# Kernel tuning notes

Measured on AMD Instinct MI355X. Metric: run time of the kernel, lower is better.

The kernel has to match this reference:

```python
import jax, jax.numpy as jnp
import numpy as np

NUM_HEADS = 12


def setup_inputs() -> dict:
    key = jax.random.key(0)
    k1, k2, k3, k4, k5 = jax.random.split(key, 5)
    B, N, C = 64, 197, 768
    P = 10  # prefix length
    H, D = NUM_HEADS, C // NUM_HEADS
    return {
        "x": jax.random.normal(k1, (B, N, C), dtype=jnp.float32),
        "prompt": jax.random.normal(k2, (B, 2, P, H, D), dtype=jnp.float32),
        "qkv_w": jax.random.normal(k3, (3 * C, C), dtype=jnp.float32) * 0.02,
        "proj_w": jax.random.normal(k4, (C, C), dtype=jnp.float32) * 0.02,
        "proj_b": jax.random.normal(k5, (C,), dtype=jnp.float32) * 0.02,
    }


def reference(x, prompt, qkv_w, proj_w, proj_b):
    B, N, C = x.shape
    H = NUM_HEADS
    D = C // H
    scale = D ** -0.5

    # qkv projection (no bias), split into per-head q, k, v: [B, H, N, D]
    qkv = jnp.einsum("bnc,fc->bnf", x, qkv_w)              # [B, N, 3C]
    qkv = qkv.reshape(B, N, 3, H, D).transpose(2, 0, 3, 1, 4)
    q, k, v = qkv[0], qkv[1], qkv[2]

    # prompt: [B, 2, P, H, D] -> [2, B, H, P, D]; concat prefix onto k, v
    p = prompt.transpose(1, 0, 3, 2, 4)
    k = jnp.concatenate([p[0], k], axis=2)                  # [B, H, P+N, D]
    v = jnp.concatenate([p[1], v], axis=2)

    attn = jnp.einsum("bhnd,bhmd->bhnm", q, k) * scale      # [B, H, N, P+N]
    attn = jax.nn.softmax(attn, axis=-1)                    # attn_drop p=0 -> identity

    out = jnp.einsum("bhnm,bhmd->bhnd", attn, v)            # [B, H, N, D]
    out = out.transpose(0, 2, 1, 3).reshape(B, N, C)
    out = jnp.einsum("bnc,oc->bno", out, proj_w) + proj_b   # proj_drop p=0 -> identity
    return out
```

## Files before the change

### kernel.cpp

```cpp
#include <hip/hip_runtime.h>
#include <hip/hip_bf16.h>
#include <stdint.h>

#define NH 12
#define DH 64
#define CC 768
#define NTOK 197
#define PFX 10
#define MKV 207
#define BB 64
#define MROWS (BB * NTOK)
#define MPAD (99 * 128)
#define NT_QKV 9
#define MT_QKV 50
#define MPAD2 (MT_QKV * 256)
#define KV_PAD 208
#define KV_PAD2 224
#define VSTRIDE 232

typedef __attribute__((__ext_vector_type__(8))) short bf16x8;
typedef __attribute__((__ext_vector_type__(4))) float f32x4;

__device__ __forceinline__ ushort f2bf(float f) {
    union { float f; uint32_t u; } x; x.f = f;
    uint32_t u = x.u;
    return (ushort)((u + 0x7fffu + ((u >> 16) & 1u)) >> 16);
}

__device__ __forceinline__ void gload_lds16(const void* g, void* l) {
    __builtin_amdgcn_global_load_lds(
        (const __attribute__((address_space(1))) void*)g,
        (__attribute__((address_space(3))) void*)l, 16, 0, 0);
}

__device__ __forceinline__ int xcd_chunked(int orig, int nwg) {
    int q = nwg >> 3, r = nwg & 7;
    int xcd = orig & 7, rem = orig >> 3;
    return (xcd < r ? xcd * (q + 1) : r * (q + 1) + (xcd - r) * q) + rem;
}

__global__ void cvt_bf16(const float* __restrict__ src, ushort* __restrict__ dst, int n4) {
    int i = blockIdx.x * 256 + threadIdx.x;
    if (i >= n4) return;
    float4 v = reinterpret_cast<const float4*>(src)[i];
    ushort4 o = make_ushort4(f2bf(v.x), f2bf(v.y), f2bf(v.z), f2bf(v.w));
    reinterpret_cast<ushort4*>(dst)[i] = o;
}

__global__ void prompt_scatter(const float* __restrict__ prompt,
                               ushort* __restrict__ kbuf, ushort* __restrict__ vt) {
    int i = blockIdx.x * 256 + threadIdx.x;
    if (i >= BB * 2 * PFX * NH * DH) return;
    int d = i & 63;
    int h = (i >> 6) % NH;
    int p = (i / (64 * NH)) % PFX;
    int s = (i / (64 * NH * PFX)) & 1;
    int b = i / (64 * NH * PFX * 2);
    ushort val = f2bf(prompt[i]);
    int bh = b * NH + h;
    if (s == 0) kbuf[(bh * KV_PAD + p) * DH + d] = val;
    else        vt[(bh * DH + d) * KV_PAD2 + p] = val;
}

#define STAGE6(kt) {                                                              \
    const int bsel = (kt) & 1; const int koff = (kt) * 64;                        \
    gload_lds16(pA[0] + koff, &lds[bsel][0][0 * 4096 + w * 512]);                 \
    gload_lds16(pA[2] + koff, &lds[bsel][0][2 * 4096 + w * 512]);                 \
    gload_lds16(pB[0] + koff, &lds[bsel][1][0 * 4096 + w * 512]);                 \
    gload_lds16(pB[1] + koff, &lds[bsel][1][1 * 4096 + w * 512]);                 \
    gload_lds16(pB[2] + koff, &lds[bsel][1][2 * 4096 + w * 512]);                 \
    gload_lds16(pB[3] + koff, &lds[bsel][1][3 * 4096 + w * 512]); }

#define STAGE2(kt) {                                                              \
    const int bsel = (kt) & 1; const int koff = (kt) * 64;                        \
    gload_lds16(pA[1] + koff, &lds[bsel][0][1 * 4096 + w * 512]);                 \
    gload_lds16(pA[3] + koff, &lds[bsel][0][3 * 4096 + w * 512]); }

#define PHASE(t, p, VMSTR, DOSTAGE) {                                             \
    if (DOSTAGE) { if ((p) == 0) STAGE6((t) + 1) else STAGE2((t) + 1) }           \
    asm volatile("s_waitcnt vmcnt(" VMSTR ")" ::: "memory");                      \
    __builtin_amdgcn_s_barrier();                                                 \
    __builtin_amdgcn_sched_barrier(0);                                            \
    const ushort* Ab = &lds[(t) & 1][0][0];                                       \
    const ushort* Bb = &lds[(t) & 1][1][0];                                       \
    bf16x8 af[4][2], bf[4][2];                                                    \
    _Pragma("unroll") for (int i = 0; i < 4; ++i)                                 \
      _Pragma("unroll") for (int ks = 0; ks < 2; ++ks)                            \
        af[i][ks] = *reinterpret_cast<const bf16x8*>(                             \
            &Ab[(wm * 128 + ((p) * 4 + i) * 16 + lr) * 64 + coff[ks]]);           \
    _Pragma("unroll") for (int n = 0; n < 4; ++n)                                 \
      _Pragma("unroll") for (int ks = 0; ks < 2; ++ks)                            \
        bf[n][ks] = *reinterpret_cast<const bf16x8*>(                             \
            &Bb[(wn * 64 + n * 16 + lr) * 64 + coff[ks]]);                        \
    __builtin_amdgcn_s_setprio(1);                                                \
    _Pragma("unroll") for (int ks = 0; ks < 2; ++ks)                              \
      _Pragma("unroll") for (int i = 0; i < 4; ++i)                               \
        _Pragma("unroll") for (int n = 0; n < 4; ++n)                             \
          acc[(p) * 4 + i][n] = __builtin_amdgcn_mfma_f32_16x16x32_bf16(          \
              af[i][ks], bf[n][ks], acc[(p) * 4 + i][n], 0, 0, 0);                \
    __builtin_amdgcn_s_setprio(0);                                                \
    __builtin_amdgcn_s_barrier();                                                 \
    __builtin_amdgcn_sched_barrier(0);                                            \
}

__global__ __launch_bounds__(512, 2) void gemm_qkv8(const ushort* __restrict__ A,
                                                    const ushort* __restrict__ Bw,
                                                    ushort* __restrict__ qbuf,
                                                    ushort* __restrict__ kbuf,
                                                    ushort* __restrict__ vt) {
    __shared__ __align__(16) ushort lds[2][2][256 * 64];
    const int tid  = threadIdx.x;
    const int lane = tid & 63;
    const int w    = tid >> 6;
    const int wm = w >> 2, wn = w & 3;
    const int g = lane >> 4, lr = lane & 15;
    const int wgid = xcd_chunked(blockIdx.x, gridDim.x);
    const int row0 = (wgid / NT_QKV) * 256;
    const int col0 = (wgid % NT_QKV) * 256;

    const int sr  = tid >> 3;
    const int scb = (((tid & 7) ^ ((tid >> 3) & 7)) << 3);
    const int lr7 = lr & 7;
    int coff[2];
    coff[0] = ((0 * 4 + g) ^ lr7) << 3;
    coff[1] = ((1 * 4 + g) ^ lr7) << 3;

    const ushort* pA[4];
    #pragma unroll
    for (int q = 0; q < 4; ++q)
        pA[q] = A + (size_t)(row0 + q * 64 + sr) * CC + scb;
    const ushort* pB[4];
    #pragma unroll
    for (int j = 0; j < 4; ++j)
        pB[j] = Bw + (size_t)(col0 + j * 64 + sr) * CC + scb;

    f32x4 acc[8][4] = {};

    STAGE6(0)
    STAGE2(0)

    for (int t = 0; t < 11; ++t) {
        PHASE(t, 0, "8", true)
        PHASE(t, 1, "8", true)
    }
    PHASE(11, 0, "2", false)
    PHASE(11, 1, "0", false)

    #pragma unroll
    for (int ni = 0; ni < 4; ++ni) {
        int f = col0 + wn * 64 + ni * 16 + lr;
        int s   = f / CC;
        int rem = f - s * CC;
        int h = rem >> 6, d = rem & 63;
        #pragma unroll
        for (int mi = 0; mi < 8; ++mi) {
            #pragma unroll
            for (int rr = 0; rr < 4; ++rr) {
                int r = row0 + wm * 128 + mi * 16 + g * 4 + rr;
                if (r >= MROWS) continue;
                int b = r / NTOK;
                int n = r - b * NTOK;
                ushort val = f2bf(acc[mi][ni][rr]);
                int bh = b * NH + h;
                if (s == 0)      qbuf[(bh * KV_PAD + n) * DH + d] = val;
                else if (s == 1) kbuf[(bh * KV_PAD + n + PFX) * DH + d] = val;
                else             vt[(bh * DH + d) * KV_PAD2 + n + PFX] = val;
            }
        }
    }
}

#define GEMM_PRE(A_, B_, KDIM, NTILES)                                               \
    __shared__ __align__(16) ushort Alds0[128 * 32];                                 \
    __shared__ __align__(16) ushort Blds0[128 * 32];                                 \
    __shared__ __align__(16) ushort Alds1[128 * 32];                                 \
    __shared__ __align__(16) ushort Blds1[128 * 32];                                 \
    const int tid  = threadIdx.x;                                                    \
    const int lane = tid & 63;                                                       \
    const int wave = tid >> 6;                                                       \
    const int wm = wave >> 1, wn = wave & 1;                                         \
    const int g = lane >> 4, lr = lane & 15;                                         \
    const int wgid = xcd_chunked(blockIdx.x, gridDim.x);                             \
    const int row0 = (wgid / (NTILES)) * 128;                                        \
    const int col0 = (wgid % (NTILES)) * 128;                                        \
    const int srow = lane >> 2;                                                      \
    const int scol = (lane & 3) * 8;                                                 \
    const ushort* gA0 = &(A_)[(size_t)(row0 + wave * 16 + srow) * (KDIM) + scol];    \
    const ushort* gA1 = gA0 + (size_t)64 * (KDIM);                                   \
    const ushort* gB0 = &(B_)[(size_t)(col0 + wave * 16 + srow) * (KDIM) + scol];    \
    const ushort* gB1 = gB0 + (size_t)64 * (KDIM);                                   \
    f32x4 acc[4][4] = {};

#define GEMM_STAGE(AB, BB_, KOFF)                                                    \
    gload_lds16(gA0 + (KOFF), &(AB)[(wave * 16) * 32]);                              \
    gload_lds16(gA1 + (KOFF), &(AB)[(64 + wave * 16) * 32]);                         \
    gload_lds16(gB0 + (KOFF), &(BB_)[(wave * 16) * 32]);                             \
    gload_lds16(gB1 + (KOFF), &(BB_)[(64 + wave * 16) * 32]);

#define GEMM_COMPUTE(AB, BB_)                                                        \
    {                                                                                \
        bf16x8 af[4], bfr[4];                                                        \
        _Pragma("unroll")                                                            \
        for (int i = 0; i < 4; ++i)                                                  \
            af[i] = *reinterpret_cast<const bf16x8*>(&(AB)[(wm * 64 + i * 16 + lr) * 32 + g * 8]); \
        _Pragma("unroll")                                                            \
        for (int i = 0; i < 4; ++i)                                                  \
            bfr[i] = *reinterpret_cast<const bf16x8*>(&(BB_)[(wn * 64 + i * 16 + lr) * 32 + g * 8]); \
        _Pragma("unroll")                                                            \
        for (int mi = 0; mi < 4; ++mi)                                               \
            _Pragma("unroll")                                                        \
            for (int ni = 0; ni < 4; ++ni)                                           \
                acc[mi][ni] = __builtin_amdgcn_mfma_f32_16x16x32_bf16(af[mi], bfr[ni], acc[mi][ni], 0, 0, 0); \
    }

#define GEMM_MAIN(A_, B_, KDIM, NTILES)                                              \
    GEMM_PRE(A_, B_, KDIM, NTILES)                                                   \
    GEMM_STAGE(Alds0, Blds0, 0)                                                      \
    __syncthreads();                                                                 \
    for (int k0 = 0; k0 < (KDIM); k0 += 64) {                                        \
        GEMM_STAGE(Alds1, Blds1, k0 + 32)                                            \
        GEMM_COMPUTE(Alds0, Blds0)                                                   \
        __syncthreads();                                                             \
        if (k0 + 64 < (KDIM)) { GEMM_STAGE(Alds0, Blds0, k0 + 64) }                  \
        GEMM_COMPUTE(Alds1, Blds1)                                                   \
        __syncthreads();                                                             \
    }

__global__ __launch_bounds__(256) void gemm_proj(const ushort* __restrict__ A,
                                                 const ushort* __restrict__ Bw,
                                                 const float* __restrict__ bias,
                                                 float* __restrict__ out) {
    GEMM_MAIN(A, Bw, CC, 6)
    #pragma unroll
    for (int ni = 0; ni < 4; ++ni) {
        int o = col0 + wn * 64 + ni * 16 + lr;
        float bs = bias[o];
        #pragma unroll
        for (int mi = 0; mi < 4; ++mi) {
            #pragma unroll
            for (int rr = 0; rr < 4; ++rr) {
                int r = row0 + wm * 64 + mi * 16 + g * 4 + rr;
                if (r >= MROWS) continue;
                out[(size_t)r * CC + o] = acc[mi][ni][rr] + bs;
            }
        }
    }
}

__global__ __launch_bounds__(512, 2) void attn_bh(const ushort* __restrict__ qbuf,
                                                  const ushort* __restrict__ kbuf,
                                                  const ushort* __restrict__ vt,
                                                  ushort* __restrict__ aout) {
    __shared__ __align__(16) ushort Klds[KV_PAD * DH];
    __shared__ __align__(16) ushort Vlds[DH * VSTRIDE];
    __shared__ __align__(16) ushort Plds[8 * 16 * VSTRIDE];
    const int tid  = threadIdx.x;
    const int lane = tid & 63;
    const int w    = tid >> 6;
    const int g = lane >> 4, lr = lane & 15;
    const int bh = blockIdx.x;
    const int b = bh / NH, h = bh - b * NH;

    const ushort* pKsrc = kbuf + (size_t)bh * KV_PAD * DH
                        + (lane >> 3) * DH + (((lane & 7) ^ (lane >> 3)) << 3);
    #pragma unroll
    for (int u = 0; u < 4; ++u) {
        int uu = w + u * 8;
        if (uu < 26) gload_lds16(pKsrc + uu * 512, &Klds[uu * 512]);
    }

    const int4* vsrc = reinterpret_cast<const int4*>(vt + (size_t)bh * DH * KV_PAD2);
    #pragma unroll
    for (int k = 0; k < 4; ++k) {
        int u = tid + 512 * k;
        if (u < DH * (KV_PAD2 / 8)) {
            int4 d = vsrc[u];
            int row  = u / (KV_PAD2 / 8);
            int colu = u - row * (KV_PAD2 / 8);
            *reinterpret_cast<int4*>(&Vlds[row * VSTRIDE + colu * 8]) = d;
        }
    }

    const ushort* Q = qbuf + (size_t)bh * KV_PAD * DH;
    const int qt0 = w, qt1 = w + 8;
    bf16x8 qf0[2], qf1[2];
    #pragma unroll
    for (int kc = 0; kc < 2; ++kc)
        qf0[kc] = *reinterpret_cast<const bf16x8*>(&Q[(qt0 * 16 + lr) * DH + kc * 32 + g * 8]);
    if (qt1 < 13) {
        #pragma unroll
        for (int kc = 0; kc < 2; ++kc)
            qf1[kc] = *reinterpret_cast<const bf16x8*>(&Q[(qt1 * 16 + lr) * DH + kc * 32 + g * 8]);
    }

    __syncthreads();

    ushort* Pw = &Plds[w * 16 * VSTRIDE];
    {
        int row = lane >> 2, col = 208 + (lane & 3) * 4;
        *reinterpret_cast<ushort4*>(&Pw[row * VSTRIDE + col]) = make_ushort4(0, 0, 0, 0);
    }

    const int kswz0 = ((0 * 4 + g) ^ (lr & 7)) << 3;
    const int kswz1 = ((1 * 4 + g) ^ (lr & 7)) << 3;
    const float cs = 0.125f * 1.4426950408889634f;

    auto process = [&](int qt, bf16x8 qfa, bf16x8 qfb) {
        f32x4 s[13];
        __builtin_amdgcn_s_setprio(1);
        #pragma unroll
        for (int t = 0; t < 13; ++t) {
            f32x4 a = {};
            bf16x8 kf0 = *reinterpret_cast<const bf16x8*>(&Klds[(t * 16 + lr) * DH + kswz0]);
            a = __builtin_amdgcn_mfma_f32_16x16x32_bf16(kf0, qfa, a, 0, 0, 0);
            bf16x8 kf1 = *reinterpret_cast<const bf16x8*>(&Klds[(t * 16 + lr) * DH + kswz1]);
            a = __builtin_amdgcn_mfma_f32_16x16x32_bf16(kf1, qfb, a, 0, 0, 0);
            s[t] = a;
        }
        __builtin_amdgcn_s_setprio(0);

        float m = -1e30f;
        #pragma unroll
        for (int t = 0; t < 13; ++t) {
            #pragma unroll
            for (int rr = 0; rr < 4; ++rr) {
                int kv = t * 16 + g * 4 + rr;
                float v = (kv < MKV) ? s[t][rr] : -1e30f;
                s[t][rr] = v;
                m = fmaxf(m, v);
            }
        }
        m = fmaxf(m, __shfl_xor(m, 16));
        m = fmaxf(m, __shfl_xor(m, 32));

        float sum = 0.f;
        #pragma unroll
        for (int t = 0; t < 13; ++t) {
            #pragma unroll
            for (int rr = 0; rr < 4; ++rr) {
                float p = exp2f((s[t][rr] - m) * cs);
                s[t][rr] = p;
                sum += p;
            }
        }
        sum += __shfl_xor(sum, 16);
        sum += __shfl_xor(sum, 32);
        float inv = 1.0f / sum;

        #pragma unroll
        for (int t = 0; t < 13; ++t) {
            #pragma unroll
            for (int rr = 0; rr < 4; ++rr)
                Pw[lr * VSTRIDE + t * 16 + g * 4 + rr] = f2bf(s[t][rr] * inv);
        }

        const int q = qt * 16 + lr;
        #pragma unroll
        for (int dt = 0; dt < 4; ++dt) {
            f32x4 o = {};
            __builtin_amdgcn_s_setprio(1);
            #pragma unroll
            for (int kc = 0; kc < 7; ++kc) {
                bf16x8 vf = *reinterpret_cast<const bf16x8*>(&Vlds[(dt * 16 + lr) * VSTRIDE + kc * 32 + g * 8]);
                bf16x8 pf = *reinterpret_cast<const bf16x8*>(&Pw[lr * VSTRIDE + kc * 32 + g * 8]);
                o = __builtin_amdgcn_mfma_f32_16x16x32_bf16(vf, pf, o, 0, 0, 0);
            }
            __builtin_amdgcn_s_setprio(0);
            if (q < NTOK) {
                ushort4 st = make_ushort4(f2bf(o[0]), f2bf(o[1]), f2bf(o[2]), f2bf(o[3]));
                int r = b * NTOK + q;
                *reinterpret_cast<ushort4*>(&aout[(size_t)r * CC + h * 64 + dt * 16 + g * 4]) = st;
            }
        }
    };

    process(qt0, qf0[0], qf0[1]);
    if (qt1 < 13) process(qt1, qf1[0], qf1[1]);
}

extern "C" void kernel_launch(void* const* d_in, const int* in_sizes, int n_in,
                              void* d_out, int out_size, void* d_ws, size_t ws_size,
                              hipStream_t stream) {
    const float* x      = (const float*)d_in[0];
    const float* prompt = (const float*)d_in[1];
    const float* qkv_w  = (const float*)d_in[2];
    const float* proj_w = (const float*)d_in[3];
    const float* proj_b = (const float*)d_in[4];
    float* out = (float*)d_out;

    char* ws = (char*)d_ws;
    ushort* Xb = (ushort*)(ws + 0);
    ushort* Wq = (ushort*)(ws + 19660800);
    ushort* Wp = (ushort*)(ws + 23199744);
    ushort* qb = (ushort*)(ws + 24379392);
    ushort* kb = (ushort*)(ws + 44826624);
    ushort* vt = (ushort*)(ws + 65273856);
    ushort* ao = (ushort*)(ws + 87293952);

    cvt_bf16<<<dim3((MROWS * CC / 4 + 255) / 256), 256, 0, stream>>>(x, Xb, MROWS * CC / 4);
    cvt_bf16<<<dim3((3 * CC * CC / 4 + 255) / 256), 256, 0, stream>>>(qkv_w, Wq, 3 * CC * CC / 4);
    cvt_bf16<<<dim3((CC * CC / 4 + 255) / 256), 256, 0, stream>>>(proj_w, Wp, CC * CC / 4);
    prompt_scatter<<<dim3((BB * 2 * PFX * NH * DH + 255) / 256), 256, 0, stream>>>(prompt, kb, vt);

    gemm_qkv8<<<dim3(MT_QKV * NT_QKV), 512, 0, stream>>>(Xb, Wq, qb, kb, vt);
    attn_bh<<<dim3(BB * NH), 512, 0, stream>>>(qb, kb, vt, ao);
    gemm_proj<<<dim3(99 * 6), 256, 0, stream>>>(ao, Wp, proj_b, out);
}
```

Measured before the change: 278.3 us.

## Write V row-major from QKV GEMM, transpose in separate kernel; coalesce attention output stores

The QKV GEMM epilogue and prompt scatter now write V in row-major [bh, n, d] layout instead of scattering strided transposed writes. A new vtrans kernel transposes V into the padded transposed layout through LDS. The attention kernel packs P stores into ushort4 writes and stages its output through LDS so each lane writes contiguous columns. This trades an extra kernel launch and one extra pass over V for more coalesced global writes. The vbuf buffer is aliased with the attention output buffer, which is safe only because vtrans finishes before attention writes to it.

```diff
diff --git a/kernel.cpp b/kernel.cpp
--- a/kernel.cpp
+++ b/kernel.cpp
@@ -48,7 +48,7 @@
 }
 
 __global__ void prompt_scatter(const float* __restrict__ prompt,
-                               ushort* __restrict__ kbuf, ushort* __restrict__ vt) {
+                               ushort* __restrict__ kbuf, ushort* __restrict__ vbuf) {
     int i = blockIdx.x * 256 + threadIdx.x;
     if (i >= BB * 2 * PFX * NH * DH) return;
     int d = i & 63;
@@ -59,7 +59,48 @@
     ushort val = f2bf(prompt[i]);
     int bh = b * NH + h;
     if (s == 0) kbuf[(bh * KV_PAD + p) * DH + d] = val;
-    else        vt[(bh * DH + d) * KV_PAD2 + p] = val;
+    else        vbuf[(bh * KV_PAD + p) * DH + d] = val;
+}
+
+__global__ __launch_bounds__(256) void vtrans(const ushort* __restrict__ vbuf,
+                                              ushort* __restrict__ vt) {
+    __shared__ __align__(16) ushort T[64][72];
+    const int tid = threadIdx.x;
+    const int bh = blockIdx.x;
+    const ushort* src = vbuf + (size_t)bh * KV_PAD * DH;
+    ushort* dst = vt + (size_t)bh * DH * KV_PAD2;
+    for (int c = 0; c < 4; ++c) {
+        const int nbase = c * 64;
+        const int nrows = (c == 3) ? 16 : 64;
+        {
+            int n = tid >> 3;
+            int db = (tid & 7) * 8;
+            if (n < nrows) {
+                int4 v0 = *reinterpret_cast<const int4*>(&src[(nbase + n) * DH + db]);
+                const ushort* p = (const ushort*)&v0;
+                #pragma unroll
+                for (int e = 0; e < 8; ++e) T[db + e][n] = p[e];
+            }
+            if (n + 32 < nrows) {
+                int4 v1 = *reinterpret_cast<const int4*>(&src[(nbase + n + 32) * DH + db]);
+                const ushort* p = (const ushort*)&v1;
+                #pragma unroll
+                for (int e = 0; e < 8; ++e) T[db + e][n + 32] = p[e];
+            }
+        }
+        __syncthreads();
+        {
+            int d = tid >> 3;
+            int nb = (tid & 7) * 8;
+            if (nb < nrows) {
+                *reinterpret_cast<int4*>(&dst[d * KV_PAD2 + nbase + nb]) =
+                    *reinterpret_cast<const int4*>(&T[d][nb]);
+                *reinterpret_cast<int4*>(&dst[(d + 32) * KV_PAD2 + nbase + nb]) =
+                    *reinterpret_cast<const int4*>(&T[d + 32][nb]);
+            }
+        }
+        __syncthreads();
+    }
 }
 
 #define STAGE6(kt) {                                                              \
@@ -107,7 +148,7 @@
                                                     const ushort* __restrict__ Bw,
                                                     ushort* __restrict__ qbuf,
                                                     ushort* __restrict__ kbuf,
-                                                    ushort* __restrict__ vt) {
+                                                    ushort* __restrict__ vbuf) {
     __shared__ __align__(16) ushort lds[2][2][256 * 64];
     const int tid  = threadIdx.x;
     const int lane = tid & 63;
@@ -164,7 +205,7 @@
                 int bh = b * NH + h;
                 if (s == 0)      qbuf[(bh * KV_PAD + n) * DH + d] = val;
                 else if (s == 1) kbuf[(bh * KV_PAD + n + PFX) * DH + d] = val;
-                else             vt[(bh * DH + d) * KV_PAD2 + n + PFX] = val;
+                else             vbuf[(bh * KV_PAD + n + PFX) * DH + d] = val;
             }
         }
     }
@@ -296,16 +337,17 @@
     __syncthreads();
 
     ushort* Pw = &Plds[w * 16 * VSTRIDE];
-    {
-        int row = lane >> 2, col = 208 + (lane & 3) * 4;
-        *reinterpret_cast<ushort4*>(&Pw[row * VSTRIDE + col]) = make_ushort4(0, 0, 0, 0);
-    }
 
     const int kswz0 = ((0 * 4 + g) ^ (lr & 7)) << 3;
     const int kswz1 = ((1 * 4 + g) ^ (lr & 7)) << 3;
     const float cs = 0.125f * 1.4426950408889634f;
 
     auto process = [&](int qt, bf16x8 qfa, bf16x8 qfb) {
+        {
+            int row = lane >> 2, col = 208 + (lane & 3) * 4;
+            *reinterpret_cast<ushort4*>(&Pw[row * VSTRIDE + col]) = make_ushort4(0, 0, 0, 0);
+        }
+
         f32x4 s[13];
         __builtin_amdgcn_s_setprio(1);
         #pragma unroll
@@ -349,28 +391,36 @@
 
         #pragma unroll
         for (int t = 0; t < 13; ++t) {
-            #pragma unroll
-            for (int rr = 0; rr < 4; ++rr)
-                Pw[lr * VSTRIDE + t * 16 + g * 4 + rr] = f2bf(s[t][rr] * inv);
-        }
-
-        const int q = qt * 16 + lr;
+            ushort4 pk = make_ushort4(f2bf(s[t][0] * inv), f2bf(s[t][1] * inv),
+                                      f2bf(s[t][2] * inv), f2bf(s[t][3] * inv));
+            *reinterpret_cast<ushort4*>(&Pw[lr * VSTRIDE + t * 16 + g * 4]) = pk;
+        }
+
+        f32x4 o[4] = {};
         #pragma unroll
         for (int dt = 0; dt < 4; ++dt) {
-            f32x4 o = {};
             __builtin_amdgcn_s_setprio(1);
             #pragma unroll
             for (int kc = 0; kc < 7; ++kc) {
                 bf16x8 vf = *reinterpret_cast<const bf16x8*>(&Vlds[(dt * 16 + lr) * VSTRIDE + kc * 32 + g * 8]);
                 bf16x8 pf = *reinterpret_cast<const bf16x8*>(&Pw[lr * VSTRIDE + kc * 32 + g * 8]);
-                o = __builtin_amdgcn_mfma_f32_16x16x32_bf16(vf, pf, o, 0, 0, 0);
+                o[dt] = __builtin_amdgcn_mfma_f32_16x16x32_bf16(vf, pf, o[dt], 0, 0, 0);
             }
             __builtin_amdgcn_s_setprio(0);
-            if (q < NTOK) {
-                ushort4 st = make_ushort4(f2bf(o[0]), f2bf(o[1]), f2bf(o[2]), f2bf(o[3]));
-                int r = b * NTOK + q;
-                *reinterpret_cast<ushort4*>(&aout[(size_t)r * CC + h * 64 + dt * 16 + g * 4]) = st;
-            }
+        }
+
+        #pragma unroll
+        for (int dt = 0; dt < 4; ++dt)
+            #pragma unroll
+            for (int rr = 0; rr < 4; ++rr)
+                Pw[(dt * 16 + g * 4 + rr) * 18 + lr] = f2bf(o[dt][rr]);
+
+        const int rbase = b * NTOK + qt * 16;
+        #pragma unroll
+        for (int q16 = 0; q16 < 16; ++q16) {
+            ushort vv = Pw[lane * 18 + q16];
+            if (qt * 16 + q16 < NTOK)
+                aout[(size_t)(rbase + q16) * CC + h * 64 + lane] = vv;
         }
     };
 
@@ -395,14 +445,16 @@
     ushort* qb = (ushort*)(ws + 24379392);
     ushort* kb = (ushort*)(ws + 44826624);
     ushort* vt = (ushort*)(ws + 65273856);
-    ushort* ao = (ushort*)(ws + 87293952);
+    ushort* vbuf = (ushort*)(ws + 87293952);
+    ushort* ao   = (ushort*)(ws + 87293952);
 
     cvt_bf16<<<dim3((MROWS * CC / 4 + 255) / 256), 256, 0, stream>>>(x, Xb, MROWS * CC / 4);
     cvt_bf16<<<dim3((3 * CC * CC / 4 + 255) / 256), 256, 0, stream>>>(qkv_w, Wq, 3 * CC * CC / 4);
     cvt_bf16<<<dim3((CC * CC / 4 + 255) / 256), 256, 0, stream>>>(proj_w, Wp, CC * CC / 4);
-    prompt_scatter<<<dim3((BB * 2 * PFX * NH * DH + 255) / 256), 256, 0, stream>>>(prompt, kb, vt);
-
-    gemm_qkv8<<<dim3(MT_QKV * NT_QKV), 512, 0, stream>>>(Xb, Wq, qb, kb, vt);
+    prompt_scatter<<<dim3((BB * 2 * PFX * NH * DH + 255) / 256), 256, 0, stream>>>(prompt, kb, vbuf);
+
+    gemm_qkv8<<<dim3(MT_QKV * NT_QKV), 512, 0, stream>>>(Xb, Wq, qb, kb, vbuf);
+    vtrans<<<dim3(BB * NH), 256, 0, stream>>>(vbuf, vt);
     attn_bh<<<dim3(BB * NH), 512, 0, stream>>>(qb, kb, vt, ao);
     gemm_proj<<<dim3(99 * 6), 256, 0, stream>>>(ao, Wp, proj_b, out);
 }
```

Measured after the change: 265.5 us. -4.6%, faster.
